# Optimization experiments

Measured on AMD Instinct MI355X. Metric: run time of the kernel, lower is better.

Reference implementation:

```python
import jax, jax.numpy as jnp
import numpy as np

N_NODES = 100000
N_EDGES = 1600000
IN_C, HID_C, OUT_C = 128, 128, 64


def setup_inputs() -> dict:
    key = jax.random.key(0)
    k = jax.random.split(key, 5)
    x = jax.random.normal(k[0], (N_NODES, IN_C), dtype=jnp.float32)
    edge_index = jax.random.randint(k[1], (2, N_EDGES), 0, N_NODES, dtype=jnp.int32)
    # Glorot-ish scaling for the GCNConv linear weights
    W1 = jax.random.normal(k[2], (IN_C, HID_C), dtype=jnp.float32) * (1.0 / np.sqrt(IN_C))
    b1 = jnp.zeros((HID_C,), dtype=jnp.float32)
    W2 = jax.random.normal(k[3], (HID_C, OUT_C), dtype=jnp.float32) * (1.0 / np.sqrt(HID_C))
    b2 = jnp.zeros((OUT_C,), dtype=jnp.float32)
    return {"x": x, "edge_index": edge_index, "W1": W1, "b1": b1, "W2": W2, "b2": b2}


def _gcn_conv(h, W, b, src, dst, deg_inv_sqrt, n):
    # h: [N, F_in] -> linear transform, then deg-normalized scatter-add over edges
    h = h @ W  # [N, F_out]
    norm = deg_inv_sqrt[src] * deg_inv_sqrt[dst]  # [E+N] (self-loops included)
    msgs = h[src] * norm[:, None]  # gather + scale
    out = jax.ops.segment_sum(msgs, dst, num_segments=n)  # scatter-add to dst
    return out + b


def reference(x, edge_index, W1, b1, W2, b2):
    n = x.shape[0]
    loops = jnp.arange(n, dtype=edge_index.dtype)
    src = jnp.concatenate([edge_index[0], loops])  # add self-loops (PyG default)
    dst = jnp.concatenate([edge_index[1], loops])
    deg = jax.ops.segment_sum(jnp.ones_like(dst, dtype=x.dtype), dst, num_segments=n)
    deg_inv_sqrt = jax.lax.rsqrt(deg)  # deg >= 1 due to self-loops

    h = _gcn_conv(x, W1, b1, src, dst, deg_inv_sqrt, n)
    h = jax.nn.relu(h)
    # F.dropout(training=False) is identity at inference
    h = _gcn_conv(h, W2, b2, src, dst, deg_inv_sqrt, n)
    return jax.nn.log_softmax(h, axis=1)
```

## Files before the change

### kernel.cpp

```cpp
#include <hip/hip_runtime.h>
#include <hip/hip_bf16.h>


typedef unsigned short ushortT;
typedef unsigned char ucharT;
typedef __attribute__((ext_vector_type(8))) short short8v;
typedef __attribute__((ext_vector_type(4))) float float4v;
typedef __attribute__((ext_vector_type(2))) float float2v;
typedef __attribute__((ext_vector_type(8))) unsigned short ushort8v;

__device__ __forceinline__ float bf2f(ushortT u) {
  union { unsigned int i; float f; } x;
  x.i = ((unsigned int)u) << 16;
  return x.f;
}

__device__ __forceinline__ ushortT f2bf(float f) {
  __hip_bfloat16 h = __float2bfloat16(f);
  return *(ushortT*)&h;
}

__device__ __forceinline__ ucharT f2fp8(float f) {
  unsigned int w = __builtin_amdgcn_cvt_pk_fp8_f32(f, f, 0, false);
  return (ucharT)(w & 0xff);
}

__device__ __forceinline__ void fp8x8_to_f32(unsigned int lo, unsigned int hi,
                                             float* f) {
  float2v p0 = __builtin_amdgcn_cvt_pk_f32_fp8(lo, false);
  float2v p1 = __builtin_amdgcn_cvt_pk_f32_fp8(lo, true);
  float2v p2 = __builtin_amdgcn_cvt_pk_f32_fp8(hi, false);
  float2v p3 = __builtin_amdgcn_cvt_pk_f32_fp8(hi, true);
  f[0] = p0[0]; f[1] = p0[1]; f[2] = p1[0]; f[3] = p1[1];
  f[4] = p2[0]; f[5] = p2[1]; f[6] = p3[0]; f[7] = p3[1];
}

__device__ __forceinline__ void fp8x4_to_f32(unsigned int w, float* f) {
  float2v p0 = __builtin_amdgcn_cvt_pk_f32_fp8(w, false);
  float2v p1 = __builtin_amdgcn_cvt_pk_f32_fp8(w, true);
  f[0] = p0[0]; f[1] = p0[1]; f[2] = p1[0]; f[3] = p1[1];
}

__device__ __forceinline__ bool probe_isbf(const void* xv) {
  const ushortT* xr = (const ushortT*)xv;
  const int lane = threadIdx.x & 63;
  float v = bf2f(xr[lane]);
  bool sane = isfinite(v) && fabsf(v) < 1e4f;
  return __ballot(sane) == ~0ull;
}

__global__ __launch_bounds__(256) void wprep_k(const void* __restrict__ W1v,
                                               const void* __restrict__ W2v,
                                               const void* __restrict__ xv,
                                               ushortT* __restrict__ Wt1,
                                               ushortT* __restrict__ Wt2) {
  const bool isbf = probe_isbf(xv);
  const int i = blockIdx.x * 256 + threadIdx.x;
  if (i < 16384) {
    int nn = i & 127, k = i >> 7;
    ushortT v = isbf ? ((const ushortT*)W1v)[k * 128 + nn]
                     : f2bf(((const float*)W1v)[k * 128 + nn]);
    Wt1[nn * 128 + k] = v;
  } else if (i < 24576) {
    int j = i - 16384;
    int nn = j & 63, k = j >> 6;
    ushortT v = isbf ? ((const ushortT*)W2v)[k * 64 + nn]
                     : f2bf(((const float*)W2v)[k * 64 + nn]);
    Wt2[nn * 128 + k] = v;
  }
}


__global__ __launch_bounds__(256) void bhist_k(const int* __restrict__ dst, int E, int B,
                                               int* __restrict__ gbc) {
  __shared__ int h[512];
  const int tid = threadIdx.x;
  for (int i = tid; i < B; i += 256) h[i] = 0;
  __syncthreads();
  const int i0 = blockIdx.x * 8192;
  const int iend = min(i0 + 8192, E);
  for (int i = i0 + tid; i < iend; i += 256) atomicAdd(&h[dst[i] >> 8], 1);
  __syncthreads();
  for (int i = tid; i < B; i += 256)
    if (h[i]) atomicAdd(&gbc[i], h[i]);
}

__global__ __launch_bounds__(256) void bscan_k(const int* __restrict__ gbc, int B,
                                               int* __restrict__ bbase,
                                               int* __restrict__ gcur) {
  __shared__ int p[256];
  const int t = threadIdx.x;
  int a = (2 * t < B) ? gbc[2 * t] : 0;
  int b = (2 * t + 1 < B) ? gbc[2 * t + 1] : 0;
  const int sum = a + b;
  p[t] = sum;
  __syncthreads();
  int run = sum;
  for (int off = 1; off < 256; off <<= 1) {
    int v = (t >= off) ? p[t - off] : 0;
    __syncthreads();
    run += v;
    p[t] = run;
    __syncthreads();
  }
  const int excl = run - sum;
  if (2 * t < B) { bbase[2 * t] = excl; gcur[2 * t] = excl; }
  if (2 * t + 1 < B) { bbase[2 * t + 1] = excl + a; gcur[2 * t + 1] = excl + a; }
}

__global__ __launch_bounds__(256) void bin_k(const int* __restrict__ srcv,
                                             const int* __restrict__ dstv, int E, int B,
                                             int* __restrict__ gcur,
                                             int* __restrict__ tmp) {
  __shared__ int hist[512];
  __shared__ int base[512];
  const int tid = threadIdx.x;
  const int i0 = blockIdx.x * 8192;
  const int iend = min(i0 + 8192, E);
  for (int i = tid; i < B; i += 256) hist[i] = 0;
  __syncthreads();
  for (int i = i0 + tid; i < iend; i += 256) atomicAdd(&hist[dstv[i] >> 8], 1);
  __syncthreads();
  for (int i = tid; i < B; i += 256) {
    int h = hist[i];
    base[i] = h ? atomicAdd(&gcur[i], h) : 0;
    hist[i] = 0;
  }
  __syncthreads();
  for (int i = i0 + tid; i < iend; i += 256) {
    int d = dstv[i];
    int s = srcv[i];
    int b = d >> 8;
    int l = atomicAdd(&hist[b], 1);
    tmp[base[b] + l] = s | ((d & 255) << 17);
  }
}

__global__ __launch_bounds__(256) void csr_k(const int* __restrict__ tmp,
                                             const int* __restrict__ bbase,
                                             const int* __restrict__ gbc, int n,
                                             int2* __restrict__ rpc,
                                             float* __restrict__ dis,
                                             int* __restrict__ col) {
  __shared__ int lhist[256];
  __shared__ int lexcl[256];
  const int b = blockIdx.x;
  const int tid = threadIdx.x;
  const int e0 = bbase[b];
  const int e1 = e0 + gbc[b];
  lhist[tid] = 0;
  __syncthreads();
  for (int i = e0 + tid; i < e1; i += 256) atomicAdd(&lhist[tmp[i] >> 17], 1);
  __syncthreads();
  const int v = lhist[tid];
  int run = v;
  lexcl[tid] = run;
  __syncthreads();
  for (int off = 1; off < 256; off <<= 1) {
    int t = (tid >= off) ? lexcl[tid - off] : 0;
    __syncthreads();
    run += t;
    lexcl[tid] = run;
    __syncthreads();
  }
  const int excl = run - v;
  const int node = (b << 8) + tid;
  if (node < n) {
    rpc[node] = make_int2(e0 + excl, v);
    dis[node] = rsqrtf((float)(v + 1));
  }
  lhist[tid] = 0;
  lexcl[tid] = excl;
  __syncthreads();
  for (int i = e0 + tid; i < e1; i += 256) {
    int p = tmp[i];
    int dloc = p >> 17;
    int s = p & 131071;
    int l = atomicAdd(&lhist[dloc], 1);
    col[e0 + lexcl[dloc] + l] = s;
  }
}

__global__ __launch_bounds__(256) void gemm1_k(const void* __restrict__ xv,
                                               const ushortT* __restrict__ Wt1,
                                               const float* __restrict__ dis,
                                               ucharT* __restrict__ Hb8, int n) {
  __shared__ ushortT sA[64 * 132];
  __shared__ ushortT sW[128 * 132];
  const bool isbf = probe_isbf(xv);
  const int tid = threadIdx.x;
  const int rb = blockIdx.x * 64;
  const int wave = tid >> 6;
  const int lane = tid & 63;
  const int m = lane & 15;
  const int quad = lane >> 4;

  if (isbf) {
    for (int i = tid; i < 2048; i += 256) {
      int r = i >> 5, c4 = (i & 31) * 4;
      ushort4 u = make_ushort4(0, 0, 0, 0);
      if (rb + r < n) u = *(const ushort4*)((const ushortT*)xv + (size_t)(rb + r) * 128 + c4);
      *(ushort4*)&sA[r * 132 + c4] = u;
    }
  } else {
    for (int i = tid; i < 2048; i += 256) {
      int r = i >> 5, c4 = (i & 31) * 4;
      float4 v = make_float4(0.f, 0.f, 0.f, 0.f);
      if (rb + r < n) v = *(const float4*)((const float*)xv + (size_t)(rb + r) * 128 + c4);
      ushort4 u;
      u.x = f2bf(v.x); u.y = f2bf(v.y); u.z = f2bf(v.z); u.w = f2bf(v.w);
      *(ushort4*)&sA[r * 132 + c4] = u;
    }
  }
  for (int i = tid; i < 4096; i += 256) {
    int nn = i >> 5, k4 = (i & 31) * 4;
    *(ushort4*)&sW[nn * 132 + k4] = *(const ushort4*)&Wt1[nn * 128 + k4];
  }
  __syncthreads();

  float4v acc[8];
#pragma unroll
  for (int t = 0; t < 8; ++t) acc[t] = (float4v)(0.f);

  const int arow = wave * 16 + m;
#pragma unroll
  for (int kc = 0; kc < 4; ++kc) {
    short8v af = *(const short8v*)&sA[arow * 132 + kc * 32 + quad * 8];
#pragma unroll
    for (int nb = 0; nb < 8; ++nb) {
      short8v bf = *(const short8v*)&sW[(nb * 16 + m) * 132 + kc * 32 + quad * 8];
      acc[nb] = __builtin_amdgcn_mfma_f32_16x16x32_bf16(af, bf, acc[nb], 0, 0, 0);
    }
  }

#pragma unroll
  for (int r = 0; r < 4; ++r) {
    int grow = rb + wave * 16 + quad * 4 + r;
    if (grow <= n) {
      float sc = (grow < n) ? dis[grow] : 0.f;
#pragma unroll
      for (int nb = 0; nb < 8; ++nb)
        Hb8[(size_t)grow * 128 + nb * 16 + m] =
            (grow < n) ? f2fp8(sc * acc[nb][r]) : (ucharT)0;
    }
  }
}

__global__ __launch_bounds__(256) void agg1_k(const ucharT* __restrict__ Hb8,
                                              const int* __restrict__ col,
                                              const int2* __restrict__ rpc,
                                              const float* __restrict__ dis,
                                              const void* __restrict__ b1v,
                                              const void* __restrict__ xv,
                                              ushortT* __restrict__ Ab, int n) {
  const bool isbf = probe_isbf(xv);
  const int tid = threadIdx.x;
  const int lane = tid & 63;
  const int wave = tid >> 6;
  const int quad = lane >> 4;
  const int m = lane & 15;
  const int c8 = m * 8;
  const int node = blockIdx.x * 16 + wave * 4 + quad;
  const bool valid = node < n;
  const int nd = valid ? node : (n - 1);

  const int2 rc = rpc[nd];
  const int start = rc.x;
  const int cnt = valid ? rc.y : 0;
  const float din = dis[nd];

  const uint2 hsp = *(const uint2*)&Hb8[((unsigned)(valid ? node : n) << 7) + (unsigned)c8];
  float b[8];
  if (isbf) {
    ushort8v bb = *(const ushort8v*)((const ushortT*)b1v + c8);
#pragma unroll
    for (int k = 0; k < 8; ++k) b[k] = bf2f(bb[k]);
  } else {
    const float* bf = (const float*)b1v + c8;
#pragma unroll
    for (int k = 0; k < 8; ++k) b[k] = bf[k];
  }

  int cmax = cnt;
  cmax = max(cmax, __shfl_xor(cmax, 16));
  cmax = max(cmax, __shfl_xor(cmax, 32));
  const int cmaxs = __builtin_amdgcn_readfirstlane(cmax);

  float2v acc[4];
#pragma unroll
  for (int k = 0; k < 4; ++k) acc[k] = (float2v)(0.f);

  for (int e = 0; e < cmaxs; e += 4) {
#pragma unroll
    for (int u = 0; u < 4; ++u) {
      const int ee = e + u;
      int s = col[start + ee];
      s = (ee < cnt) ? s : n;
      const uint2 h = *(const uint2*)&Hb8[((unsigned)s << 7) + (unsigned)c8];
      acc[0] += __builtin_amdgcn_cvt_pk_f32_fp8(h.x, false);
      acc[1] += __builtin_amdgcn_cvt_pk_f32_fp8(h.x, true);
      acc[2] += __builtin_amdgcn_cvt_pk_f32_fp8(h.y, false);
      acc[3] += __builtin_amdgcn_cvt_pk_f32_fp8(h.y, true);
    }
  }

  if (valid) {
    float hs[8];
    fp8x8_to_f32(hsp.x, hsp.y, hs);
    ushort8v o;
#pragma unroll
    for (int k = 0; k < 4; ++k) {
      o[2 * k]     = f2bf(fmaxf(fmaf(din, acc[k][0] + hs[2 * k],     b[2 * k]),     0.f));
      o[2 * k + 1] = f2bf(fmaxf(fmaf(din, acc[k][1] + hs[2 * k + 1], b[2 * k + 1]), 0.f));
    }
    *(ushort8v*)&Ab[(size_t)node * 128 + c8] = o;
  }
}

__global__ __launch_bounds__(256) void gemm2_k(const ushortT* __restrict__ Ab,
                                               const ushortT* __restrict__ Wt2,
                                               const float* __restrict__ dis,
                                               ucharT* __restrict__ H2b8, int n) {
  __shared__ ushortT sA[64 * 132];
  __shared__ ushortT sW[64 * 132];
  const int tid = threadIdx.x;
  const int rb = blockIdx.x * 64;
  const int wave = tid >> 6;
  const int lane = tid & 63;
  const int m = lane & 15;
  const int quad = lane >> 4;

  for (int i = tid; i < 2048; i += 256) {
    int r = i >> 5, c4 = (i & 31) * 4;
    ushort4 u = make_ushort4(0, 0, 0, 0);
    if (rb + r < n) u = *(const ushort4*)&Ab[(size_t)(rb + r) * 128 + c4];
    *(ushort4*)&sA[r * 132 + c4] = u;
  }
  for (int i = tid; i < 2048; i += 256) {
    int nn = i >> 5, k4 = (i & 31) * 4;
    *(ushort4*)&sW[nn * 132 + k4] = *(const ushort4*)&Wt2[nn * 128 + k4];
  }
  __syncthreads();

  float4v acc[4];
#pragma unroll
  for (int t = 0; t < 4; ++t) acc[t] = (float4v)(0.f);

  const int arow = wave * 16 + m;
#pragma unroll
  for (int kc = 0; kc < 4; ++kc) {
    short8v af = *(const short8v*)&sA[arow * 132 + kc * 32 + quad * 8];
#pragma unroll
    for (int nb = 0; nb < 4; ++nb) {
      short8v bf = *(const short8v*)&sW[(nb * 16 + m) * 132 + kc * 32 + quad * 8];
      acc[nb] = __builtin_amdgcn_mfma_f32_16x16x32_bf16(af, bf, acc[nb], 0, 0, 0);
    }
  }

#pragma unroll
  for (int r = 0; r < 4; ++r) {
    int grow = rb + wave * 16 + quad * 4 + r;
    if (grow <= n) {
      float sc = (grow < n) ? dis[grow] : 0.f;
#pragma unroll
      for (int nb = 0; nb < 4; ++nb)
        H2b8[(size_t)grow * 64 + nb * 16 + m] =
            (grow < n) ? f2fp8(sc * acc[nb][r]) : (ucharT)0;
    }
  }
}

__global__ __launch_bounds__(256) void agg2_k(const ucharT* __restrict__ H2b8,
                                              const int* __restrict__ col,
                                              const int2* __restrict__ rpc,
                                              const float* __restrict__ dis,
                                              const void* __restrict__ b2v,
                                              const void* __restrict__ xv,
                                              void* __restrict__ outv, int n) {
  const bool isbf = probe_isbf(xv);
  const int tid = threadIdx.x;
  const int lane = tid & 63;
  const int wave = tid >> 6;
  const int quad = lane >> 4;
  const int m = lane & 15;
  const int c4 = m * 4;
  const int node = blockIdx.x * 16 + wave * 4 + quad;
  const bool valid = node < n;
  const int nd = valid ? node : (n - 1);

  const int2 rc = rpc[nd];
  const int start = rc.x;
  const int cnt = valid ? rc.y : 0;
  const float din = dis[nd];

  const unsigned int hsp =
      *(const unsigned int*)&H2b8[((unsigned)(valid ? node : n) << 6) + (unsigned)c4];
  float b[4];
  if (isbf) {
    ushort4 bb = *(const ushort4*)((const ushortT*)b2v + c4);
    b[0] = bf2f(bb.x); b[1] = bf2f(bb.y); b[2] = bf2f(bb.z); b[3] = bf2f(bb.w);
  } else {
    const float* bf = (const float*)b2v + c4;
#pragma unroll
    for (int k = 0; k < 4; ++k) b[k] = bf[k];
  }

  int cmax = cnt;
  cmax = max(cmax, __shfl_xor(cmax, 16));
  cmax = max(cmax, __shfl_xor(cmax, 32));
  const int cmaxs = __builtin_amdgcn_readfirstlane(cmax);

  float2v acc[2];
  acc[0] = (float2v)(0.f);
  acc[1] = (float2v)(0.f);

  for (int e = 0; e < cmaxs; e += 4) {
#pragma unroll
    for (int u = 0; u < 4; ++u) {
      const int ee = e + u;
      int s = col[start + ee];
      s = (ee < cnt) ? s : n;
      const unsigned int h = *(const unsigned int*)&H2b8[((unsigned)s << 6) + (unsigned)c4];
      acc[0] += __builtin_amdgcn_cvt_pk_f32_fp8(h, false);
      acc[1] += __builtin_amdgcn_cvt_pk_f32_fp8(h, true);
    }
  }

  float hs[4];
  fp8x4_to_f32(hsp, hs);
  float v[4];
  v[0] = fmaf(din, acc[0][0] + hs[0], b[0]);
  v[1] = fmaf(din, acc[0][1] + hs[1], b[1]);
  v[2] = fmaf(din, acc[1][0] + hs[2], b[2]);
  v[3] = fmaf(din, acc[1][1] + hs[3], b[3]);

  float mx = fmaxf(fmaxf(v[0], v[1]), fmaxf(v[2], v[3]));
  for (int off = 1; off < 16; off <<= 1) mx = fmaxf(mx, __shfl_xor(mx, off));
  float ssum = __expf(v[0] - mx) + __expf(v[1] - mx) + __expf(v[2] - mx) + __expf(v[3] - mx);
  for (int off = 1; off < 16; off <<= 1) ssum += __shfl_xor(ssum, off);
  const float lse = mx + __logf(ssum);

  if (valid) {
    if (isbf) {
      ushort4 o;
      o.x = f2bf(v[0] - lse); o.y = f2bf(v[1] - lse);
      o.z = f2bf(v[2] - lse); o.w = f2bf(v[3] - lse);
      *(ushort4*)((__hip_bfloat16*)outv + (size_t)node * 64 + c4) = o;
    } else {
      float4 o = make_float4(v[0] - lse, v[1] - lse, v[2] - lse, v[3] - lse);
      *(float4*)((float*)outv + (size_t)node * 64 + c4) = o;
    }
  }
}


extern "C" void kernel_launch(void* const* d_in, const int* in_sizes, int n_in,
                              void* d_out, int out_size, void* d_ws, size_t ws_size,
                              hipStream_t stream) {
  const void* x  = d_in[0];
  const int*  ei = (const int*)d_in[1];
  const void* W1 = d_in[2];
  const void* b1 = d_in[3];
  const void* W2 = d_in[4];
  const void* b2 = d_in[5];

  const int n = in_sizes[0] / 128;
  const int E = in_sizes[1] / 2;
  const int B = (n + 255) >> 8;
  const int* srcv = ei;
  const int* dstv = ei + E;

  char* p = (char*)d_ws;
  auto alloc = [&](size_t bytes) {
    char* q = p;
    p += (bytes + 255) & ~(size_t)255;
    return q;
  };
  ucharT* Hb8 = (ucharT*)alloc((size_t)(n + 1) * 128);
  ucharT* H2b8 = (ucharT*)alloc((size_t)(n + 1) * 64);
  ushortT* Ab = (ushortT*)alloc((size_t)n * 128 * 2);
  float* dis = (float*)alloc((size_t)n * 4);
  int2* rpc = (int2*)alloc((size_t)n * 8);
  int* gbc = (int*)alloc(512 * 4);
  int* bbase = (int*)alloc(512 * 4);
  int* gcur = (int*)alloc(512 * 4);
  ushortT* Wt1 = (ushortT*)alloc(16384 * 2);
  ushortT* Wt2 = (ushortT*)alloc(8192 * 2);
  int* tmp = (int*)alloc((size_t)E * 4);
  int* col = (int*)alloc(((size_t)E + 4096) * 4);

  (void)hipMemsetAsync(gbc, 0, 512 * sizeof(int), stream);

  const int gChunks = (E + 8191) / 8192;

  wprep_k<<<96, 256, 0, stream>>>(W1, W2, x, Wt1, Wt2);
  bhist_k<<<gChunks, 256, 0, stream>>>(dstv, E, B, gbc);
  bscan_k<<<1, 256, 0, stream>>>(gbc, B, bbase, gcur);
  bin_k<<<gChunks, 256, 0, stream>>>(srcv, dstv, E, B, gcur, tmp);
  csr_k<<<B, 256, 0, stream>>>(tmp, bbase, gbc, n, rpc, dis, col);

  gemm1_k<<<(n + 63) / 64, 256, 0, stream>>>(x, Wt1, dis, Hb8, n);
  agg1_k<<<(n + 15) / 16, 256, 0, stream>>>(Hb8, col, rpc, dis, b1, x, Ab, n);
  gemm2_k<<<(n + 63) / 64, 256, 0, stream>>>(Ab, Wt2, dis, H2b8, n);
  agg2_k<<<(n + 15) / 16, 256, 0, stream>>>(H2b8, col, rpc, dis, b2, x, d_out, n);
}
```

Before: 256.8 us.

## Load GEMM A-fragments directly from global memory and enlarge blocks to 128 rows

Both node-feature GEMM kernels no longer stage the A tile in shared memory. Each lane now reads its MFMA A-fragment straight from global memory, with the row clamped to n-1. Blocks grow to 512 threads covering 128 rows, so the weight tile is loaded into LDS half as often and the LDS round trip for activations is removed. Global reads are now 16-32 byte strided per lane rather than fully coalesced, and the grid is sized (n+128)/128, which keeps the extra padding row n written.

```diff
diff --git a/kernel.cpp b/kernel.cpp
--- a/kernel.cpp
+++ b/kernel.cpp
@@ -181,61 +181,63 @@
   }
 }
 
-__global__ __launch_bounds__(256) void gemm1_k(const void* __restrict__ xv,
+__global__ __launch_bounds__(512) void gemm1_k(const void* __restrict__ xv,
                                                const ushortT* __restrict__ Wt1,
                                                const float* __restrict__ dis,
                                                ucharT* __restrict__ Hb8, int n) {
-  __shared__ ushortT sA[64 * 132];
   __shared__ ushortT sW[128 * 132];
   const bool isbf = probe_isbf(xv);
   const int tid = threadIdx.x;
-  const int rb = blockIdx.x * 64;
+  for (int i = tid; i < 4096; i += 512) {
+    int nn = i >> 5, k4 = (i & 31) * 4;
+    *(ushort4*)&sW[nn * 132 + k4] = *(const ushort4*)&Wt1[nn * 128 + k4];
+  }
+  __syncthreads();
+
   const int wave = tid >> 6;
   const int lane = tid & 63;
   const int m = lane & 15;
   const int quad = lane >> 4;
+  const int row = blockIdx.x * 128 + wave * 16 + m;
+  const int rowc = min(row, n - 1);
+
+  float4v acc[8];
+#pragma unroll
+  for (int t = 0; t < 8; ++t) acc[t] = (float4v)(0.f);
 
   if (isbf) {
-    for (int i = tid; i < 2048; i += 256) {
-      int r = i >> 5, c4 = (i & 31) * 4;
-      ushort4 u = make_ushort4(0, 0, 0, 0);
-      if (rb + r < n) u = *(const ushort4*)((const ushortT*)xv + (size_t)(rb + r) * 128 + c4);
-      *(ushort4*)&sA[r * 132 + c4] = u;
+    const ushortT* xp = (const ushortT*)xv + (size_t)rowc * 128 + quad * 8;
+#pragma unroll
+    for (int kc = 0; kc < 4; ++kc) {
+      short8v af = *(const short8v*)(xp + kc * 32);
+#pragma unroll
+      for (int nb = 0; nb < 8; ++nb) {
+        short8v bf = *(const short8v*)&sW[(nb * 16 + m) * 132 + kc * 32 + quad * 8];
+        acc[nb] = __builtin_amdgcn_mfma_f32_16x16x32_bf16(af, bf, acc[nb], 0, 0, 0);
+      }
     }
   } else {
-    for (int i = tid; i < 2048; i += 256) {
-      int r = i >> 5, c4 = (i & 31) * 4;
-      float4 v = make_float4(0.f, 0.f, 0.f, 0.f);
-      if (rb + r < n) v = *(const float4*)((const float*)xv + (size_t)(rb + r) * 128 + c4);
-      ushort4 u;
-      u.x = f2bf(v.x); u.y = f2bf(v.y); u.z = f2bf(v.z); u.w = f2bf(v.w);
-      *(ushort4*)&sA[r * 132 + c4] = u;
-    }
-  }
-  for (int i = tid; i < 4096; i += 256) {
-    int nn = i >> 5, k4 = (i & 31) * 4;
-    *(ushort4*)&sW[nn * 132 + k4] = *(const ushort4*)&Wt1[nn * 128 + k4];
-  }
-  __syncthreads();
-
-  float4v acc[8];
-#pragma unroll
-  for (int t = 0; t < 8; ++t) acc[t] = (float4v)(0.f);
-
-  const int arow = wave * 16 + m;
-#pragma unroll
-  for (int kc = 0; kc < 4; ++kc) {
-    short8v af = *(const short8v*)&sA[arow * 132 + kc * 32 + quad * 8];
-#pragma unroll
-    for (int nb = 0; nb < 8; ++nb) {
-      short8v bf = *(const short8v*)&sW[(nb * 16 + m) * 132 + kc * 32 + quad * 8];
-      acc[nb] = __builtin_amdgcn_mfma_f32_16x16x32_bf16(af, bf, acc[nb], 0, 0, 0);
+    const float* xp = (const float*)xv + (size_t)rowc * 128 + quad * 8;
+#pragma unroll
+    for (int kc = 0; kc < 4; ++kc) {
+      float4 lo = *(const float4*)(xp + kc * 32);
+      float4 hi = *(const float4*)(xp + kc * 32 + 4);
+      short8v af;
+      af[0] = (short)f2bf(lo.x); af[1] = (short)f2bf(lo.y);
+      af[2] = (short)f2bf(lo.z); af[3] = (short)f2bf(lo.w);
+      af[4] = (short)f2bf(hi.x); af[5] = (short)f2bf(hi.y);
+      af[6] = (short)f2bf(hi.z); af[7] = (short)f2bf(hi.w);
+#pragma unroll
+      for (int nb = 0; nb < 8; ++nb) {
+        short8v bf = *(const short8v*)&sW[(nb * 16 + m) * 132 + kc * 32 + quad * 8];
+        acc[nb] = __builtin_amdgcn_mfma_f32_16x16x32_bf16(af, bf, acc[nb], 0, 0, 0);
+      }
     }
   }
 
 #pragma unroll
   for (int r = 0; r < 4; ++r) {
-    int grow = rb + wave * 16 + quad * 4 + r;
+    int grow = blockIdx.x * 128 + wave * 16 + quad * 4 + r;
     if (grow <= n) {
       float sc = (grow < n) ? dis[grow] : 0.f;
 #pragma unroll
@@ -317,39 +319,33 @@
   }
 }
 
-__global__ __launch_bounds__(256) void gemm2_k(const ushortT* __restrict__ Ab,
+__global__ __launch_bounds__(512) void gemm2_k(const ushortT* __restrict__ Ab,
                                                const ushortT* __restrict__ Wt2,
                                                const float* __restrict__ dis,
                                                ucharT* __restrict__ H2b8, int n) {
-  __shared__ ushortT sA[64 * 132];
   __shared__ ushortT sW[64 * 132];
   const int tid = threadIdx.x;
-  const int rb = blockIdx.x * 64;
+  for (int i = tid; i < 2048; i += 512) {
+    int nn = i >> 5, k4 = (i & 31) * 4;
+    *(ushort4*)&sW[nn * 132 + k4] = *(const ushort4*)&Wt2[nn * 128 + k4];
+  }
+  __syncthreads();
+
   const int wave = tid >> 6;
   const int lane = tid & 63;
   const int m = lane & 15;
   const int quad = lane >> 4;
-
-  for (int i = tid; i < 2048; i += 256) {
-    int r = i >> 5, c4 = (i & 31) * 4;
-    ushort4 u = make_ushort4(0, 0, 0, 0);
-    if (rb + r < n) u = *(const ushort4*)&Ab[(size_t)(rb + r) * 128 + c4];
-    *(ushort4*)&sA[r * 132 + c4] = u;
-  }
-  for (int i = tid; i < 2048; i += 256) {
-    int nn = i >> 5, k4 = (i & 31) * 4;
-    *(ushort4*)&sW[nn * 132 + k4] = *(const ushort4*)&Wt2[nn * 128 + k4];
-  }
-  __syncthreads();
+  const int row = blockIdx.x * 128 + wave * 16 + m;
+  const int rowc = min(row, n - 1);
 
   float4v acc[4];
 #pragma unroll
   for (int t = 0; t < 4; ++t) acc[t] = (float4v)(0.f);
 
-  const int arow = wave * 16 + m;
+  const ushortT* ap = Ab + (size_t)rowc * 128 + quad * 8;
 #pragma unroll
   for (int kc = 0; kc < 4; ++kc) {
-    short8v af = *(const short8v*)&sA[arow * 132 + kc * 32 + quad * 8];
+    short8v af = *(const short8v*)(ap + kc * 32);
 #pragma unroll
     for (int nb = 0; nb < 4; ++nb) {
       short8v bf = *(const short8v*)&sW[(nb * 16 + m) * 132 + kc * 32 + quad * 8];
@@ -359,7 +355,7 @@
 
 #pragma unroll
   for (int r = 0; r < 4; ++r) {
-    int grow = rb + wave * 16 + quad * 4 + r;
+    int grow = blockIdx.x * 128 + wave * 16 + quad * 4 + r;
     if (grow <= n) {
       float sc = (grow < n) ? dis[grow] : 0.f;
 #pragma unroll
@@ -499,8 +495,8 @@
   bin_k<<<gChunks, 256, 0, stream>>>(srcv, dstv, E, B, gcur, tmp);
   csr_k<<<B, 256, 0, stream>>>(tmp, bbase, gbc, n, rpc, dis, col);
 
-  gemm1_k<<<(n + 63) / 64, 256, 0, stream>>>(x, Wt1, dis, Hb8, n);
+  gemm1_k<<<(n + 128) / 128, 512, 0, stream>>>(x, Wt1, dis, Hb8, n);
   agg1_k<<<(n + 15) / 16, 256, 0, stream>>>(Hb8, col, rpc, dis, b1, x, Ab, n);
-  gemm2_k<<<(n + 63) / 64, 256, 0, stream>>>(Ab, Wt2, dis, H2b8, n);
+  gemm2_k<<<(n + 128) / 128, 512, 0, stream>>>(Ab, Wt2, dis, H2b8, n);
   agg2_k<<<(n + 15) / 16, 256, 0, stream>>>(H2b8, col, rpc, dis, b2, x, d_out, n);
 }
```

Measured after the change: 238.4 us. 1.08x faster.
